# Performance work log

Hardware: AMD Instinct MI355X
Metric: run time of the kernel (lower is better)

## Reference

```python
import jax, jax.numpy as jnp
import numpy as np
from jax import lax

DIM = 256
HEADS = 8
SR = 4
EPS = 1e-5
SCALE = (DIM // HEADS) ** -0.5


def _dwconv(x, wgt, stride, pad):
    # x: (B,C,H,W), wgt: (C,1,kh,kw) depthwise
    return lax.conv_general_dilated(
        x, wgt, (stride, stride), [(pad, pad), (pad, pad)],
        feature_group_count=x.shape[1],
        dimension_numbers=("NCHW", "OIHW", "NCHW"))


def _bn(x, g, b, m, v):
    # eval-mode batchnorm folded to per-channel scale/shift
    s = g / jnp.sqrt(v + EPS)
    return x * s[:, None, None] + (b - m * s)[:, None, None]


def setup_inputs() -> dict:
    key = jax.random.key(0)
    ks = jax.random.split(key, 16)
    b, h, w = 8, 64, 64
    c = DIM
    n = h * w

    def rn(k, shape, s=0.05):
        return jax.random.normal(k, shape, jnp.float32) * s

    return dict(
        x=jax.random.normal(ks[0], (b, n, c), jnp.float32),
        h=h, w=w,
        Wq=rn(ks[1], (c, c)), bq=rn(ks[2], (c,)),
        Wkv=rn(ks[3], (2 * c, c)), bkv=rn(ks[4], (2 * c,)),
        sr_w1=rn(ks[5], (c, 1, SR + 3, SR + 3), 0.1),
        bn1_gamma=1.0 + rn(ks[6], (c,)), bn1_beta=rn(ks[7], (c,)),
        bn1_mean=rn(ks[8], (c,)), bn1_var=jnp.abs(1.0 + rn(ks[9], (c,))),
        sr_w2=1.0 + rn(ks[10], (c,), 0.2),  # 1x1 depthwise conv == per-channel scale
        bn2_gamma=1.0 + rn(ks[11], (c,)), bn2_beta=rn(ks[12], (c,)),
        bn2_mean=rn(ks[13], (c,)), bn2_var=jnp.abs(1.0 + rn(ks[14], (c,))),
        local_w=rn(ks[15], (c, 1, 3, 3), 0.1),
        local_b=jnp.zeros((c,), jnp.float32),
    )


def reference(x, h, w, Wq, bq, Wkv, bkv, sr_w1, bn1_gamma, bn1_beta, bn1_mean,
              bn1_var, sr_w2, bn2_gamma, bn2_beta, bn2_mean, bn2_var,
              local_w, local_b):
    b, n, c = x.shape
    hd = c // HEADS
    xi = x.transpose(0, 2, 1).reshape(b, c, h, w)  # (b,c,h,w)

    # q projection (1x1 conv == channel matmul)
    q = jnp.einsum("bchw,dc->bdhw", xi, Wq) + bq[None, :, None, None]
    q = q.reshape(b, HEADS, hd, n).transpose(0, 1, 3, 2)  # (b,H,n,hd)

    # spatial reduction: dwconv7 s4 + BN + GELU + dw1x1 + BN
    kv = _dwconv(xi, sr_w1, SR, (SR + 3) // 2)
    kv = _bn(kv, bn1_gamma, bn1_beta, bn1_mean, bn1_var)
    kv = jax.nn.gelu(kv, approximate=False)
    kv = kv * sr_w2[None, :, None, None]
    kv = _bn(kv, bn2_gamma, bn2_beta, bn2_mean, bn2_var)

    # residual local depthwise 3x3 conv
    kv = _dwconv(kv, local_w, 1, 1) + local_b[None, :, None, None] + kv

    # kv projection and split
    kvp = jnp.einsum("bchw,dc->bdhw", kv, Wkv) + bkv[None, :, None, None]
    k_, v_ = jnp.split(kvp, 2, axis=1)
    m = k_.shape[2] * k_.shape[3]
    k_ = k_.reshape(b, HEADS, hd, m)                       # (b,H,hd,m)
    v_ = v_.reshape(b, HEADS, hd, m).transpose(0, 1, 3, 2)  # (b,H,m,hd)

    attn = jax.nn.softmax(jnp.einsum("bhnd,bhdm->bhnm", q, k_) * SCALE, axis=-1)
    out = jnp.einsum("bhnm,bhmd->bhnd", attn, v_)           # (b,H,n,hd)
    out = out.transpose(0, 1, 3, 2).reshape(b, c, n).transpose(0, 2, 1)
    return out
```

## Files before the change

kernel.cpp:

```cpp
#include <hip/hip_runtime.h>
#include <math.h>

typedef __bf16 bf16;
typedef bf16 bf16x4 __attribute__((ext_vector_type(4)));
typedef bf16 bf16x8 __attribute__((ext_vector_type(8)));
typedef float f32x4 __attribute__((ext_vector_type(4)));

static_assert(sizeof(bf16x8) == 16, "bf16x8 must be 16B");

#define QSCALE (0.17677669529663687f * 1.4426950408889634f)

__device__ __forceinline__ f32x4 mfma16(bf16x8 a, bf16x8 b, f32x4 c) {
  return __builtin_amdgcn_mfma_f32_16x16x32_bf16(a, b, c, 0, 0, 0);
}

__global__ __launch_bounds__(256) void k_cvt(
    const float* __restrict__ Wq, const float* __restrict__ Wkv,
    const float* __restrict__ w7, bf16* __restrict__ Wqb,
    bf16* __restrict__ Wkvb, float* __restrict__ w7t) {
  const int tid = threadIdx.x;
  const int blk = blockIdx.x;
  if (blk < 96) {
    const float* src;
    bf16* dst;
    if (blk < 32) {
      const int idx = blk * 256 + tid;
      src = Wq + (size_t)idx * 8;
      dst = Wqb + (size_t)idx * 8;
    } else {
      const int idx = (blk - 32) * 256 + tid;
      src = Wkv + (size_t)idx * 8;
      dst = Wkvb + (size_t)idx * 8;
    }
    const float4 a = ((const float4*)src)[0];
    const float4 b = ((const float4*)src)[1];
    bf16x8 r;
    r[0] = (bf16)a.x; r[1] = (bf16)a.y; r[2] = (bf16)a.z; r[3] = (bf16)a.w;
    r[4] = (bf16)b.x; r[5] = (bf16)b.y; r[6] = (bf16)b.z; r[7] = (bf16)b.w;
    *(bf16x8*)dst = r;
  } else {
    const int c = tid;
    #pragma unroll
    for (int tap = 0; tap < 49; tap++)
      w7t[tap * 256 + c] = w7[c * 49 + tap];
  }
}

__global__ __launch_bounds__(256) void k_srq(
    const float* __restrict__ x, const float* __restrict__ w7t,
    const float* __restrict__ g1, const float* __restrict__ b1,
    const float* __restrict__ m1, const float* __restrict__ v1,
    const float* __restrict__ sw2,
    const float* __restrict__ g2, const float* __restrict__ b2,
    const float* __restrict__ m2, const float* __restrict__ v2,
    bf16* __restrict__ kv1,
    const bf16* __restrict__ Wqb, const float* __restrict__ bq,
    bf16* __restrict__ q_ws) {
  const int nq = gridDim.x / 3;
  const int tid = threadIdx.x;

  if (blockIdx.x < (unsigned)nq) {
    __shared__ bf16 xs[32 * 264];
    const int wv = tid >> 6, lane = tid & 63;
    const int qd = lane >> 4, l15 = lane & 15;
    const size_t rowbase = (size_t)blockIdx.x * 32;

    #pragma unroll
    for (int it = 0; it < 4; it++) {
      const int idx = it * 256 + tid;
      const int lr = idx >> 5, pos = idx & 31;
      const float* src = x + (rowbase + lr) * 256 + pos * 8;
      const float4 a = ((const float4*)src)[0];
      const float4 b = ((const float4*)src)[1];
      bf16x8 r;
      r[0] = (bf16)a.x; r[1] = (bf16)a.y; r[2] = (bf16)a.z; r[3] = (bf16)a.w;
      r[4] = (bf16)b.x; r[5] = (bf16)b.y; r[6] = (bf16)b.z; r[7] = (bf16)b.w;
      *(bf16x8*)(xs + lr * 264 + pos * 8) = r;
    }
    __syncthreads();

    f32x4 acc0[4], acc1[4];
    #pragma unroll
    for (int dt = 0; dt < 4; dt++) {
      acc0[dt] = (f32x4){0.f, 0.f, 0.f, 0.f};
      acc1[dt] = (f32x4){0.f, 0.f, 0.f, 0.f};
    }
    #pragma unroll 2
    for (int kc = 0; kc < 8; kc++) {
      const bf16x8 a0 = *(const bf16x8*)(xs + l15 * 264 + kc * 32 + qd * 8);
      const bf16x8 a1 = *(const bf16x8*)(xs + (16 + l15) * 264 + kc * 32 + qd * 8);
      #pragma unroll
      for (int dt = 0; dt < 4; dt++) {
        const int d = wv * 64 + dt * 16 + l15;
        const bf16x8 bb = *(const bf16x8*)(Wqb + (size_t)d * 256 + kc * 32 + qd * 8);
        acc0[dt] = mfma16(a0, bb, acc0[dt]);
        acc1[dt] = mfma16(a1, bb, acc1[dt]);
      }
    }
    #pragma unroll
    for (int dt = 0; dt < 4; dt++) {
      const int d = wv * 64 + dt * 16 + l15;
      const float bias = bq[d];
      const int h = d >> 5, dl = d & 31;
      #pragma unroll
      for (int r = 0; r < 4; r++) {
        const size_t row0 = rowbase + qd * 4 + r;
        const size_t row1 = rowbase + 16 + qd * 4 + r;
        q_ws[(((row0 >> 12) * 8 + h) * 4096 + (row0 & 4095)) * 32 + dl] =
            (bf16)((acc0[dt][r] + bias) * QSCALE);
        q_ws[(((row1 >> 12) * 8 + h) * 4096 + (row1 & 4095)) * 32 + dl] =
            (bf16)((acc1[dt][r] + bias) * QSCALE);
      }
    }
  } else {
    __shared__ float part[4][256];
    const int team = tid >> 6, g = tid & 63;
    const int c0 = g * 4;
    const int blk = blockIdx.x - nq;
    const int b = blk & 7, m = blk >> 3;
    const int oy = m >> 4, ox = m & 15;

    float4 xv[13], wv[13];
    float msk[13];
    #pragma unroll
    for (int j = 0; j < 13; j++) {
      const int tap = team + j * 4;
      const int ky = tap / 7, kx = tap - ky * 7;
      const int iy = oy * 4 - 3 + ky, ix = ox * 4 - 3 + kx;
      msk[j] = (tap < 49 && iy >= 0 && iy < 64 && ix >= 0 && ix < 64) ? 1.f : 0.f;
      const int iyc = iy < 0 ? 0 : (iy > 63 ? 63 : iy);
      const int ixc = ix < 0 ? 0 : (ix > 63 ? 63 : ix);
      const int tc = tap > 48 ? 48 : tap;
      xv[j] = *(const float4*)(x + ((size_t)b * 4096 + iyc * 64 + ixc) * 256 + c0);
      wv[j] = *(const float4*)(w7t + tc * 256 + c0);
    }
    float a0 = 0.f, a1 = 0.f, a2 = 0.f, a3 = 0.f;
    #pragma unroll
    for (int j = 0; j < 13; j++) {
      a0 += xv[j].x * wv[j].x * msk[j];
      a1 += xv[j].y * wv[j].y * msk[j];
      a2 += xv[j].z * wv[j].z * msk[j];
      a3 += xv[j].w * wv[j].w * msk[j];
    }
    *(f32x4*)&part[team][c0] = (f32x4){a0, a1, a2, a3};
    __syncthreads();
    const int c = tid;
    float y = part[0][c] + part[1][c] + part[2][c] + part[3][c];
    float s = g1[c] / sqrtf(v1[c] + 1e-5f);
    y = y * s + (b1[c] - m1[c] * s);
    y = 0.5f * y * (1.f + erff(y * 0.70710678118654752f));
    y *= sw2[c];
    s = g2[c] / sqrtf(v2[c] + 1e-5f);
    y = y * s + (b2[c] - m2[c] * s);
    kv1[((size_t)b * 256 + m) * 256 + c] = (bf16)y;
  }
}

__global__ __launch_bounds__(256) void k_localkv(
    const bf16* __restrict__ kv1, const float* __restrict__ w3,
    const float* __restrict__ lb, const bf16* __restrict__ Wkvb,
    const float* __restrict__ bkv, bf16* __restrict__ k_a,
    bf16* __restrict__ v_b) {
  __shared__ bf16 halo[3][10][256];
  __shared__ float rows[8][256];
  const int c = threadIdx.x;
  const int mt = blockIdx.x;
  const int part = blockIdx.y;
  const int b = blockIdx.z;
  const int oy = mt >> 1, o0 = (mt & 1) * 8;

  #pragma unroll
  for (int p = 0; p < 30; p++) {
    const int dy = p / 10, xi = p - dy * 10;
    const int iy = oy - 1 + dy, ix = o0 - 1 + xi;
    const bool ok = (iy >= 0 && iy < 16 && ix >= 0 && ix < 16);
    const int iyc = ok ? iy : 0, ixc = ok ? ix : 0;
    const bf16 v = kv1[((size_t)b * 256 + iyc * 16 + ixc) * 256 + c];
    halo[dy][xi][c] = ok ? v : (bf16)0.f;
  }
  float w3f[9];
  #pragma unroll
  for (int t = 0; t < 9; t++) w3f[t] = w3[c * 9 + t];
  const float lbf = lb[c];
  __syncthreads();

  #pragma unroll
  for (int r = 0; r < 8; r++) {
    float acc = lbf + (float)halo[1][r + 1][c];
    #pragma unroll
    for (int ky = 0; ky < 3; ky++)
      #pragma unroll
      for (int kx = 0; kx < 3; kx++)
        acc += (float)halo[ky][r + kx][c] * w3f[ky * 3 + kx];
    rows[r][c] = acc;
  }
  __syncthreads();

  const int tid = c;
  const size_t wrow = (size_t)tid + (part ? 256 : 0);
  float accs[8] = {0};
  for (int oc = 0; oc < 32; oc++) {
    const bf16x8 w0 = *(const bf16x8*)(Wkvb + wrow * 256 + oc * 8);
    float wf0[8];
    #pragma unroll
    for (int j = 0; j < 8; j++) wf0[j] = (float)w0[j];
    #pragma unroll
    for (int r = 0; r < 8; r++) {
      const float4* rp = (const float4*)&rows[r][oc * 8];
      const float4 ra = rp[0], rb = rp[1];
      const float rv[8] = {ra.x, ra.y, ra.z, ra.w, rb.x, rb.y, rb.z, rb.w};
      #pragma unroll
      for (int j = 0; j < 8; j++) accs[r] += wf0[j] * rv[j];
    }
  }
  const float bias = bkv[wrow];
  const int h = tid >> 5, d = tid & 31;
  if (part == 0) {
    #pragma unroll
    for (int r = 0; r < 8; r++) {
      const int m = (oy * 16 + o0) + r;
      k_a[(((size_t)b * 8 + h) * 256 + m) * 32 + d] = (bf16)(accs[r] + bias);
    }
  } else {
    #pragma unroll
    for (int r = 0; r < 8; r++) {
      const int m = (oy * 16 + o0) + r;
      v_b[(((size_t)b * 8 + h) * 32 + d) * 256 + m] = (bf16)(accs[r] + bias);
    }
  }
}

__global__ __launch_bounds__(256) void k_attn(
    const bf16* __restrict__ q_ws, const bf16* __restrict__ k_a,
    const bf16* __restrict__ v_b, float* __restrict__ out) {
  const int tid = threadIdx.x;
  const int wv = tid >> 6, lane = tid & 63;
  const int qd = lane >> 4, l15 = lane & 15;
  const int b = blockIdx.z, h = blockIdx.y;
  const int bh = b * 8 + h;
  const int n_base = blockIdx.x * 256 + wv * 64;

  const bf16* qb = q_ws + ((size_t)bh * 4096 + n_base) * 32;
  bf16x8 qf[4];
  #pragma unroll
  for (int qi = 0; qi < 4; qi++)
    qf[qi] = *(const bf16x8*)(qb + (size_t)(qi * 16 + l15) * 32 + qd * 8);

  const bf16* kb = k_a + (size_t)bh * 256 * 32;
  const bf16* vb = v_b + (size_t)bh * 32 * 256;

  f32x4 acc[4][2];
  float lr[4] = {0.f, 0.f, 0.f, 0.f};
  #pragma unroll
  for (int qi = 0; qi < 4; qi++) {
    acc[qi][0] = (f32x4){0.f, 0.f, 0.f, 0.f};
    acc[qi][1] = (f32x4){0.f, 0.f, 0.f, 0.f};
  }
  const int kperm = 8 * (l15 >> 2) + (l15 & 3);

  bf16x8 ka0 = *(const bf16x8*)(kb + (size_t)kperm * 32 + qd * 8);
  bf16x8 ka1 = *(const bf16x8*)(kb + (size_t)(kperm + 4) * 32 + qd * 8);
  bf16x8 va0 = *(const bf16x8*)(vb + (size_t)l15 * 256 + qd * 8);
  bf16x8 va1 = *(const bf16x8*)(vb + (size_t)(16 + l15) * 256 + qd * 8);

  for (int ch = 0; ch < 8; ch++) {
    const int cn = (ch < 7 ? ch + 1 : 7) * 32;
    const bf16x8 nk0 = *(const bf16x8*)(kb + (size_t)(cn + kperm) * 32 + qd * 8);
    const bf16x8 nk1 = *(const bf16x8*)(kb + (size_t)(cn + kperm + 4) * 32 + qd * 8);
    const bf16x8 nv0 = *(const bf16x8*)(vb + (size_t)l15 * 256 + cn + qd * 8);
    const bf16x8 nv1 = *(const bf16x8*)(vb + (size_t)(16 + l15) * 256 + cn + qd * 8);
    const f32x4 z = (f32x4){0.f, 0.f, 0.f, 0.f};
    #pragma unroll
    for (int qi = 0; qi < 4; qi++) {
      f32x4 s0 = mfma16(ka0, qf[qi], z);
      f32x4 s1 = mfma16(ka1, qf[qi], z);
      float p[8], ls = 0.f;
      #pragma unroll
      for (int j = 0; j < 4; j++) {
        p[j] = __builtin_amdgcn_exp2f(fminf(s0[j], 80.f));
        p[4 + j] = __builtin_amdgcn_exp2f(fminf(s1[j], 80.f));
      }
      #pragma unroll
      for (int j = 0; j < 8; j++) ls += p[j];
      lr[qi] += ls;
      bf16x8 pb;
      #pragma unroll
      for (int j = 0; j < 8; j++) pb[j] = (bf16)p[j];
      acc[qi][0] = mfma16(va0, pb, acc[qi][0]);
      acc[qi][1] = mfma16(va1, pb, acc[qi][1]);
    }
    ka0 = nk0; ka1 = nk1; va0 = nv0; va1 = nv1;
  }
  #pragma unroll
  for (int qi = 0; qi < 4; qi++) {
    float l = lr[qi];
    l += __shfl_xor(l, 16, 64);
    l += __shfl_xor(l, 32, 64);
    const float inv = 1.f / l;
    const int nn = n_base + qi * 16 + l15;
    float* ob = out + (size_t)(b * 4096 + nn) * 256 + h * 32;
    #pragma unroll
    for (int t = 0; t < 2; t++) {
      *(float4*)(ob + t * 16 + qd * 4) =
          (float4){acc[qi][t][0] * inv, acc[qi][t][1] * inv,
                   acc[qi][t][2] * inv, acc[qi][t][3] * inv};
    }
  }
}

extern "C" void kernel_launch(void* const* d_in, const int* in_sizes, int n_in,
                              void* d_out, int out_size, void* d_ws, size_t ws_size,
                              hipStream_t stream) {
  const float* x      = (const float*)d_in[0];
  const float* Wq     = (const float*)d_in[3];
  const float* bq     = (const float*)d_in[4];
  const float* Wkv    = (const float*)d_in[5];
  const float* bkv    = (const float*)d_in[6];
  const float* sr_w1  = (const float*)d_in[7];
  const float* bn1_g  = (const float*)d_in[8];
  const float* bn1_b  = (const float*)d_in[9];
  const float* bn1_m  = (const float*)d_in[10];
  const float* bn1_v  = (const float*)d_in[11];
  const float* sw2    = (const float*)d_in[12];
  const float* bn2_g  = (const float*)d_in[13];
  const float* bn2_b  = (const float*)d_in[14];
  const float* bn2_m  = (const float*)d_in[15];
  const float* bn2_v  = (const float*)d_in[16];
  const float* lw     = (const float*)d_in[17];
  const float* lb     = (const float*)d_in[18];

  const int B = in_sizes[0] / (4096 * 256);

  bf16* Wqb  = (bf16*)d_ws;
  bf16* Wkvb = Wqb + 65536;
  float* w7t = (float*)(Wkvb + 131072);
  bf16* kv1  = (bf16*)(w7t + 12544);
  bf16* k_a  = kv1 + (size_t)B * 256 * 256;
  bf16* v_b  = k_a + (size_t)B * 8 * 256 * 32;
  bf16* q_ws = v_b + (size_t)B * 8 * 32 * 256;

  k_cvt<<<dim3(97), 256, 0, stream>>>(Wq, Wkv, sr_w1, Wqb, Wkvb, w7t);
  k_srq<<<dim3(B * 384), 256, 0, stream>>>(x, w7t, bn1_g, bn1_b, bn1_m, bn1_v,
                                           sw2, bn2_g, bn2_b, bn2_m, bn2_v, kv1,
                                           Wqb, bq, q_ws);
  k_localkv<<<dim3(32, 2, B), 256, 0, stream>>>(kv1, lw, lb, Wkvb, bkv, k_a, v_b);
  k_attn<<<dim3(16, 8, B), 256, 0, stream>>>(q_ws, k_a, v_b, (float*)d_out);
}
```

Baseline: 184.3 us.

## Split strided 7x7 depthwise conv into row partials plus vertical-reduce kernel

The spatial-reduction conv used to gather all 49 taps per output pixel from x, so overlapping windows re-read the same input. Now each block handles one input row and reads it once. It computes horizontal 7-tap partial sums for the up to two output rows that input row feeds, and writes them to an fp32 scratch buffer H. A new k_fin kernel sums the 7 vertical partials, then applies BN, GELU, scale and BN to produce kv1. This cuts redundant x gathers, but adds a sizable fp32 intermediate write and read, plus an extra kernel launch.

```diff
diff --git a/kernel.cpp b/kernel.cpp
--- a/kernel.cpp
+++ b/kernel.cpp
@@ -48,15 +48,9 @@
 
 __global__ __launch_bounds__(256) void k_srq(
     const float* __restrict__ x, const float* __restrict__ w7t,
-    const float* __restrict__ g1, const float* __restrict__ b1,
-    const float* __restrict__ m1, const float* __restrict__ v1,
-    const float* __restrict__ sw2,
-    const float* __restrict__ g2, const float* __restrict__ b2,
-    const float* __restrict__ m2, const float* __restrict__ v2,
-    bf16* __restrict__ kv1,
     const bf16* __restrict__ Wqb, const float* __restrict__ bq,
-    bf16* __restrict__ q_ws) {
-  const int nq = gridDim.x / 3;
+    bf16* __restrict__ q_ws, float* __restrict__ H) {
+  const int nq = (gridDim.x / 3) * 2;
   const int tid = threadIdx.x;
 
   if (blockIdx.x < (unsigned)nq) {
@@ -113,46 +107,85 @@
       }
     }
   } else {
-    __shared__ float part[4][256];
-    const int team = tid >> 6, g = tid & 63;
-    const int c0 = g * 4;
     const int blk = blockIdx.x - nq;
-    const int b = blk & 7, m = blk >> 3;
-    const int oy = m >> 4, ox = m & 15;
-
-    float4 xv[13], wv[13];
-    float msk[13];
-    #pragma unroll
-    for (int j = 0; j < 13; j++) {
-      const int tap = team + j * 4;
-      const int ky = tap / 7, kx = tap - ky * 7;
-      const int iy = oy * 4 - 3 + ky, ix = ox * 4 - 3 + kx;
-      msk[j] = (tap < 49 && iy >= 0 && iy < 64 && ix >= 0 && ix < 64) ? 1.f : 0.f;
-      const int iyc = iy < 0 ? 0 : (iy > 63 ? 63 : iy);
-      const int ixc = ix < 0 ? 0 : (ix > 63 ? 63 : ix);
-      const int tc = tap > 48 ? 48 : tap;
-      xv[j] = *(const float4*)(x + ((size_t)b * 4096 + iyc * 64 + ixc) * 256 + c0);
-      wv[j] = *(const float4*)(w7t + tc * 256 + c0);
-    }
-    float a0 = 0.f, a1 = 0.f, a2 = 0.f, a3 = 0.f;
-    #pragma unroll
-    for (int j = 0; j < 13; j++) {
-      a0 += xv[j].x * wv[j].x * msk[j];
-      a1 += xv[j].y * wv[j].y * msk[j];
-      a2 += xv[j].z * wv[j].z * msk[j];
-      a3 += xv[j].w * wv[j].w * msk[j];
-    }
-    *(f32x4*)&part[team][c0] = (f32x4){a0, a1, a2, a3};
-    __syncthreads();
-    const int c = tid;
-    float y = part[0][c] + part[1][c] + part[2][c] + part[3][c];
-    float s = g1[c] / sqrtf(v1[c] + 1e-5f);
-    y = y * s + (b1[c] - m1[c] * s);
+    const int b = blk >> 6, iy = blk & 63;
+    const int w = tid >> 6, lane = tid & 63;
+    const int c4 = lane * 4;
+    const int r1 = (iy + 3) & 3;
+    const bool has2 = (r1 <= 2);
+
+    float4 wr0[7], wr1[7];
+    #pragma unroll
+    for (int kx = 0; kx < 7; kx++) {
+      wr0[kx] = *(const float4*)(w7t + (r1 * 7 + kx) * 256 + c4);
+      wr1[kx] = has2 ? *(const float4*)(w7t + ((r1 + 4) * 7 + kx) * 256 + c4)
+                     : (float4){0.f, 0.f, 0.f, 0.f};
+    }
+    const float* xrow = x + ((size_t)b * 4096 + (size_t)iy * 64) * 256;
+
+    float4 a0[4], a1[4];
+    #pragma unroll
+    for (int o = 0; o < 4; o++) {
+      a0[o] = (float4){0.f, 0.f, 0.f, 0.f};
+      a1[o] = (float4){0.f, 0.f, 0.f, 0.f};
+    }
+    #pragma unroll
+    for (int o = 0; o < 4; o++) {
+      const int ox = w * 4 + o;
+      #pragma unroll
+      for (int kx = 0; kx < 7; kx++) {
+        const int px = 4 * ox - 3 + kx;
+        if (px >= 0) {
+          const float4 xv = *(const float4*)(xrow + (size_t)px * 256 + c4);
+          a0[o].x += wr0[kx].x * xv.x; a0[o].y += wr0[kx].y * xv.y;
+          a0[o].z += wr0[kx].z * xv.z; a0[o].w += wr0[kx].w * xv.w;
+          a1[o].x += wr1[kx].x * xv.x; a1[o].y += wr1[kx].y * xv.y;
+          a1[o].z += wr1[kx].z * xv.z; a1[o].w += wr1[kx].w * xv.w;
+        }
+      }
+    }
+    float* hb = H + (((size_t)(b * 64 + iy) * 2) * 16) * 256;
+    #pragma unroll
+    for (int o = 0; o < 4; o++) {
+      const int ox = w * 4 + o;
+      *(float4*)(hb + (size_t)ox * 256 + c4) = a0[o];
+      *(float4*)(hb + (size_t)(16 + ox) * 256 + c4) = a1[o];
+    }
+  }
+}
+
+__global__ __launch_bounds__(256) void k_fin(
+    const float* __restrict__ H,
+    const float* __restrict__ g1, const float* __restrict__ b1,
+    const float* __restrict__ m1, const float* __restrict__ v1,
+    const float* __restrict__ sw2,
+    const float* __restrict__ g2, const float* __restrict__ b2,
+    const float* __restrict__ m2, const float* __restrict__ v2,
+    bf16* __restrict__ kv1) {
+  const int c = threadIdx.x;
+  const int xh = blockIdx.x, oy = blockIdx.y, b = blockIdx.z;
+
+  const float s1 = g1[c] / sqrtf(v1[c] + 1e-5f);
+  const float t1 = b1[c] - m1[c] * s1;
+  const float s2 = g2[c] / sqrtf(v2[c] + 1e-5f);
+  const float t2 = b2[c] - m2[c] * s2;
+  const float sw = sw2[c];
+
+  #pragma unroll
+  for (int o = 0; o < 8; o++) {
+    const int ox = xh * 8 + o;
+    float y = 0.f;
+    #pragma unroll
+    for (int r = 0; r < 7; r++) {
+      const int iy = 4 * oy - 3 + r;
+      if (iy >= 0)
+        y += H[((size_t)((b * 64 + iy) * 2 + (r >> 2)) * 16 + ox) * 256 + c];
+    }
+    y = y * s1 + t1;
     y = 0.5f * y * (1.f + erff(y * 0.70710678118654752f));
-    y *= sw2[c];
-    s = g2[c] / sqrtf(v2[c] + 1e-5f);
-    y = y * s + (b2[c] - m2[c] * s);
-    kv1[((size_t)b * 256 + m) * 256 + c] = (bf16)y;
+    y *= sw;
+    y = y * s2 + t2;
+    kv1[((size_t)b * 256 + oy * 16 + ox) * 256 + c] = (bf16)y;
   }
 }
 
@@ -338,11 +371,12 @@
   bf16* k_a  = kv1 + (size_t)B * 256 * 256;
   bf16* v_b  = k_a + (size_t)B * 8 * 256 * 32;
   bf16* q_ws = v_b + (size_t)B * 8 * 32 * 256;
+  float* H   = (float*)(q_ws + (size_t)B * 8 * 4096 * 32);
 
   k_cvt<<<dim3(97), 256, 0, stream>>>(Wq, Wkv, sr_w1, Wqb, Wkvb, w7t);
-  k_srq<<<dim3(B * 384), 256, 0, stream>>>(x, w7t, bn1_g, bn1_b, bn1_m, bn1_v,
-                                           sw2, bn2_g, bn2_b, bn2_m, bn2_v, kv1,
-                                           Wqb, bq, q_ws);
+  k_srq<<<dim3(B * 192), 256, 0, stream>>>(x, w7t, Wqb, bq, q_ws, H);
+  k_fin<<<dim3(2, 16, B), 256, 0, stream>>>(H, bn1_g, bn1_b, bn1_m, bn1_v,
+                                            sw2, bn2_g, bn2_b, bn2_m, bn2_v, kv1);
   k_localkv<<<dim3(32, 2, B), 256, 0, stream>>>(kv1, lw, lb, Wkvb, bkv, k_a, v_b);
   k_attn<<<dim3(16, 8, B), 256, 0, stream>>>(q_ws, k_a, v_b, (float*)d_out);
 }
```

After: 200.7 us. 1.09x slower.
